# Optimization experiments

Measured on AMD Instinct MI355X. Metric: run time of the kernel, lower is better.

## Reference

```python
import jax, jax.numpy as jnp
import numpy as np

H = 32   # hidden_dim
D = 3    # input_dim
NM, NF = 16, 64
ME, FE = 4, 2


def setup_inputs() -> dict:
    key = jax.random.key(0)
    ks = jax.random.split(key, 12)
    B, T = 16384, 1024
    s_ih = 1.0 / np.sqrt(H)
    inp = {
        "x": jax.random.normal(ks[0], (B, T, D), dtype=jnp.float32),
        "mat_idx": jax.random.randint(ks[1], (B,), 0, NM, dtype=jnp.int32),
        "freq_idx": jax.random.randint(ks[2], (B,), 0, NF, dtype=jnp.int32),
        # LSTM params (PyTorch layout: gates [i, f, g, o] stacked)
        "W_ih": jax.random.uniform(ks[3], (4 * H, D), jnp.float32, -s_ih, s_ih),
        "W_hh": jax.random.uniform(ks[4], (4 * H, H), jnp.float32, -s_ih, s_ih),
        "b_ih": jax.random.uniform(ks[5], (4 * H,), jnp.float32, -s_ih, s_ih),
        "b_hh": jax.random.uniform(ks[6], (4 * H,), jnp.float32, -s_ih, s_ih),
        "mat_emb": jax.random.normal(ks[7], (NM, ME), dtype=jnp.float32),
        "freq_emb": jax.random.normal(ks[8], (NF, FE), dtype=jnp.float32),
        "fc_w": jax.random.uniform(ks[9], (1, H + ME + FE), jnp.float32, -s_ih, s_ih),
        "fc_b": jax.random.uniform(ks[10], (1,), jnp.float32, -s_ih, s_ih),
    }
    return inp


def _lstm_last(x, W_ih, W_hh, b_ih, b_hh):
    # x: [B, T, D] -> last hidden state h_T: [B, H]
    B = x.shape[0]
    # Precompute input projections for all timesteps: [T, B, 4H]
    xg = jnp.einsum("btd,gd->tbg", x, W_ih) + (b_ih + b_hh)

    def step(carry, xg_t):
        h, c = carry
        gates = xg_t + h @ W_hh.T  # [B, 4H]
        i, f, g, o = jnp.split(gates, 4, axis=-1)
        i, f, o = jax.nn.sigmoid(i), jax.nn.sigmoid(f), jax.nn.sigmoid(o)
        g = jnp.tanh(g)
        c = f * c + i * g
        h = o * jnp.tanh(c)
        return (h, c), None

    h0 = jnp.zeros((B, H), dtype=x.dtype)
    (h, _), _ = jax.lax.scan(step, (h0, h0), xg)
    return h


def reference(x, mat_idx, freq_idx, W_ih, W_hh, b_ih, b_hh,
              mat_emb, freq_emb, fc_w, fc_b):
    last = _lstm_last(x, W_ih, W_hh, b_ih, b_hh)          # [B, H]
    feat = jnp.concatenate(
        [last, mat_emb[mat_idx], freq_emb[freq_idx]], axis=-1)  # [B, H+ME+FE]
    return (feat @ fc_w.T + fc_b)[:, 0]                   # [B]
```

## Files before the change

kernel.cpp:

```cpp
#include <hip/hip_runtime.h>
#include <hip/hip_bf16.h>

#define H 32
#define DCT 32
#define BT 32
#define HPADB 80
#define XLDS_BYTES (DCT*32*16)
#define HLDS_OFF XLDS_BYTES
#define SMEM_BYTES (XLDS_BYTES + 32*HPADB)

typedef __attribute__((ext_vector_type(8))) short bfrag;
typedef __attribute__((ext_vector_type(4))) float ffrag;

__device__ __forceinline__ unsigned short f2bf(float f) {
  union { float f; unsigned u; } v; v.f = f;
  unsigned r = v.u + 0x7FFFu + ((v.u >> 16) & 1u);
  return (unsigned short)(r >> 16);
}

__device__ __forceinline__ float sigmoid_f(float x) {
  float e = __builtin_amdgcn_exp2f(x * -1.44269504f);
  return __builtin_amdgcn_rcpf(1.0f + e);
}
__device__ __forceinline__ float tanh_f(float x) {
  float e = __builtin_amdgcn_exp2f(x * 2.88539008f);
  return 1.0f - 2.0f * __builtin_amdgcn_rcpf(e + 1.0f);
}

__global__ __launch_bounds__(256, 2) void lstm_kernel(
    const float* __restrict__ x, const int* __restrict__ mat_idx,
    const int* __restrict__ freq_idx, const float* __restrict__ W_ih,
    const float* __restrict__ W_hh, const float* __restrict__ b_ih,
    const float* __restrict__ b_hh, const float* __restrict__ mat_emb,
    const float* __restrict__ freq_emb, const float* __restrict__ fc_w,
    const float* __restrict__ fc_b, float* __restrict__ out, int T)
{
  __shared__ __align__(16) unsigned char smem[SMEM_BYTES];
  const int tid  = threadIdx.x;
  const int lane = tid & 63;
  const int wid  = tid >> 6;
  const int mtile = wid & 1;
  const int h16   = wid >> 1;
  const int q    = lane >> 4;
  const int c16  = lane & 15;
  const int hid  = h16*16 + c16;
  const int b0   = blockIdx.x * BT;

  for (int i = tid; i < SMEM_BYTES/4; i += 256) ((unsigned*)smem)[i] = 0u;

  bfrag fw[4]; bfrag fx[4];
  #pragma unroll
  for (int g = 0; g < 4; ++g) {
    const int col = g*32 + hid;
    const float* wr = W_hh + col*H + q*8;
    #pragma unroll
    for (int j = 0; j < 8; ++j) fw[g][j] = (short)f2bf(wr[j]);
    #pragma unroll
    for (int j = 0; j < 8; ++j) {
      float v = 0.0f;
      if (q == 0) {
        if (j < 3)       v = W_ih[col*3 + j];
        else if (j == 3) v = b_ih[col] + b_hh[col];
      }
      fx[g][j] = (short)f2bf(v);
    }
  }

  const unsigned h_rd = HLDS_OFF + (unsigned)(mtile*16 + c16)*HPADB + q*16;
  const unsigned x_rd = (unsigned)(mtile*16 + c16)*16;

  float cc[4] = {0.f,0.f,0.f,0.f};
  float hh[4] = {0.f,0.f,0.f,0.f};

  const int srow = tid >> 3, ssub = tid & 7;
  const float* xsrc = x + (size_t)(b0 + srow) * (size_t)T * 3;

  for (int t0 = 0; t0 < T; t0 += DCT) {
    __syncthreads();
    {
      const float* p = xsrc + (size_t)(t0 + ssub*4) * 3;
      float v[12];
      #pragma unroll
      for (int u = 0; u < 12; ++u) v[u] = p[u];
      #pragma unroll
      for (int u = 0; u < 4; ++u) {
        unsigned w0 = (unsigned)f2bf(v[u*3+0]) | ((unsigned)f2bf(v[u*3+1]) << 16);
        unsigned w1 = (unsigned)f2bf(v[u*3+2]) | (0x3F80u << 16);
        unsigned* dst = (unsigned*)(smem + (unsigned)((ssub*4+u)*32 + srow)*16);
        dst[0] = w0; dst[1] = w1;
      }
    }
    __syncthreads();

    for (int tl = 0; tl < DCT; ++tl) {
      bfrag ah = *(const bfrag*)(smem + h_rd);
      bfrag ax = *(const bfrag*)(smem + (unsigned)tl*512 + x_rd);
      ffrag acc[4] = {};
      #pragma unroll
      for (int g = 0; g < 4; ++g) {
        acc[g] = __builtin_amdgcn_mfma_f32_16x16x32_bf16(ax, fx[g], acc[g], 0,0,0);
        acc[g] = __builtin_amdgcn_mfma_f32_16x16x32_bf16(ah, fw[g], acc[g], 0,0,0);
      }
      __syncthreads();
      #pragma unroll
      for (int r = 0; r < 4; ++r) {
        float ig = sigmoid_f(acc[0][r]);
        float fg = sigmoid_f(acc[1][r]);
        float gg = tanh_f(acc[2][r]);
        float og = sigmoid_f(acc[3][r]);
        float c  = fg*cc[r] + ig*gg;
        cc[r] = c;
        float h = og * tanh_f(c);
        hh[r] = h;
        *(unsigned short*)(smem + HLDS_OFF +
            (unsigned)(mtile*16 + q*4 + r)*HPADB + (unsigned)hid*2) = f2bf(h);
      }
      __syncthreads();
    }
  }

  __syncthreads();
  float* hout = (float*)smem;
  #pragma unroll
  for (int r = 0; r < 4; ++r)
    hout[(mtile*16 + q*4 + r)*H + hid] = hh[r];
  __syncthreads();
  if (tid < BT) {
    const int b = b0 + tid;
    float acc = fc_b[0];
    const float* hv = hout + tid*H;
    #pragma unroll
    for (int k = 0; k < H; ++k) acc += hv[k]*fc_w[k];
    const int mi = mat_idx[b];
    #pragma unroll
    for (int e = 0; e < 4; ++e) acc += mat_emb[mi*4+e]*fc_w[H+e];
    const int fi = freq_idx[b];
    #pragma unroll
    for (int e = 0; e < 2; ++e) acc += freq_emb[fi*2+e]*fc_w[H+4+e];
    out[b] = acc;
  }
}

extern "C" void kernel_launch(void* const* d_in, const int* in_sizes, int n_in,
                              void* d_out, int out_size, void* d_ws, size_t ws_size,
                              hipStream_t stream) {
  const float* x        = (const float*)d_in[0];
  const int*   mat_idx  = (const int*)d_in[1];
  const int*   freq_idx = (const int*)d_in[2];
  const float* W_ih     = (const float*)d_in[3];
  const float* W_hh     = (const float*)d_in[4];
  const float* b_ih     = (const float*)d_in[5];
  const float* b_hh     = (const float*)d_in[6];
  const float* mat_emb  = (const float*)d_in[7];
  const float* freq_emb = (const float*)d_in[8];
  const float* fc_w     = (const float*)d_in[9];
  const float* fc_b     = (const float*)d_in[10];
  float* out = (float*)d_out;
  const int B = in_sizes[1];
  const int T = in_sizes[0] / (B * 3);
  dim3 grid(B / BT), block(256);
  hipLaunchKernelGGL(lstm_kernel, grid, block, 0, stream,
                     x, mat_idx, freq_idx, W_ih, W_hh, b_ih, b_hh,
                     mat_emb, freq_emb, fc_w, fc_b, out, T);
}
```

Before: 923.7 us.

## Double-buffer LSTM hidden state, halve batch tile, prescale gate weights

Hidden-state LDS is double-buffered so each recurrent step needs one barrier instead of two. The batch tile drops from 32 to 16 rows with 128-thread blocks, doubling the number of independent blocks to hide the serial step latency. Gate weights and biases are pre-multiplied by the exp2 scale factors so the sigmoid and tanh evaluations skip a multiply per element. Prescaling before bf16 rounding slightly changes numerics, and smaller blocks reuse the weight fragments less.

```diff
diff --git a/kernel.cpp b/kernel.cpp
--- a/kernel.cpp
+++ b/kernel.cpp
@@ -3,11 +3,12 @@
 
 #define H 32
 #define DCT 32
-#define BT 32
+#define BT 16
 #define HPADB 80
-#define XLDS_BYTES (DCT*32*16)
+#define XLDS_BYTES (DCT*BT*16)
 #define HLDS_OFF XLDS_BYTES
-#define SMEM_BYTES (XLDS_BYTES + 32*HPADB)
+#define HBUF (BT*HPADB)
+#define SMEM_BYTES (XLDS_BYTES + 2*HBUF)
 
 typedef __attribute__((ext_vector_type(8))) short bfrag;
 typedef __attribute__((ext_vector_type(4))) float ffrag;
@@ -18,16 +19,45 @@
   return (unsigned short)(r >> 16);
 }
 
-__device__ __forceinline__ float sigmoid_f(float x) {
-  float e = __builtin_amdgcn_exp2f(x * -1.44269504f);
-  return __builtin_amdgcn_rcpf(1.0f + e);
+__device__ __forceinline__ float sig_pre(float s) {
+  return __builtin_amdgcn_rcpf(1.0f + __builtin_amdgcn_exp2f(s));
 }
-__device__ __forceinline__ float tanh_f(float x) {
-  float e = __builtin_amdgcn_exp2f(x * 2.88539008f);
-  return 1.0f - 2.0f * __builtin_amdgcn_rcpf(e + 1.0f);
+__device__ __forceinline__ float tanh_pre(float s) {
+  return 1.0f - 2.0f * __builtin_amdgcn_rcpf(1.0f + __builtin_amdgcn_exp2f(s));
 }
 
-__global__ __launch_bounds__(256, 2) void lstm_kernel(
+__device__ __forceinline__ void lstm_step(unsigned char* smem,
+    unsigned x_off, unsigned rd_off, unsigned wr_off,
+    const bfrag* fx, const bfrag* fw, ffrag fzero, float* cc, float* hh)
+{
+  bfrag ah = *(const bfrag*)(smem + rd_off);
+  bfrag ax = *(const bfrag*)(smem + x_off);
+  ffrag a0 = __builtin_amdgcn_mfma_f32_16x16x32_bf16(ax, fx[0], fzero, 0,0,0);
+  ffrag a1 = __builtin_amdgcn_mfma_f32_16x16x32_bf16(ax, fx[1], fzero, 0,0,0);
+  ffrag a2 = __builtin_amdgcn_mfma_f32_16x16x32_bf16(ax, fx[2], fzero, 0,0,0);
+  ffrag a3 = __builtin_amdgcn_mfma_f32_16x16x32_bf16(ax, fx[3], fzero, 0,0,0);
+  a0 = __builtin_amdgcn_mfma_f32_16x16x32_bf16(ah, fw[0], a0, 0,0,0);
+  a1 = __builtin_amdgcn_mfma_f32_16x16x32_bf16(ah, fw[1], a1, 0,0,0);
+  a2 = __builtin_amdgcn_mfma_f32_16x16x32_bf16(ah, fw[2], a2, 0,0,0);
+  a3 = __builtin_amdgcn_mfma_f32_16x16x32_bf16(ah, fw[3], a3, 0,0,0);
+  #pragma unroll
+  for (int r = 0; r < 4; ++r) {
+    float i_ = sig_pre(a0[r]);
+    float f_ = sig_pre(a1[r]);
+    float tg = tanh_pre(a2[r]);
+    float o_ = sig_pre(a3[r]);
+    float c  = f_*cc[r] + i_*tg;
+    cc[r] = c;
+    float h = o_ * tanh_pre(c * 2.885390082f);
+    hh[r] = h;
+    __hip_bfloat16 hb = __float2bfloat16(h);
+    *(unsigned short*)(smem + wr_off + (unsigned)r*HPADB) =
+        __builtin_bit_cast(unsigned short, hb);
+  }
+  __syncthreads();
+}
+
+__global__ __launch_bounds__(128, 2) void lstm_kernel(
     const float* __restrict__ x, const int* __restrict__ mat_idx,
     const int* __restrict__ freq_idx, const float* __restrict__ W_ih,
     const float* __restrict__ W_hh, const float* __restrict__ b_ih,
@@ -38,45 +68,49 @@
   __shared__ __align__(16) unsigned char smem[SMEM_BYTES];
   const int tid  = threadIdx.x;
   const int lane = tid & 63;
-  const int wid  = tid >> 6;
-  const int mtile = wid & 1;
-  const int h16   = wid >> 1;
+  const int h16  = tid >> 6;
   const int q    = lane >> 4;
   const int c16  = lane & 15;
   const int hid  = h16*16 + c16;
   const int b0   = blockIdx.x * BT;
 
-  for (int i = tid; i < SMEM_BYTES/4; i += 256) ((unsigned*)smem)[i] = 0u;
+  for (int i = tid; i < SMEM_BYTES/4; i += 128) ((unsigned*)smem)[i] = 0u;
 
   bfrag fw[4]; bfrag fx[4];
   #pragma unroll
   for (int g = 0; g < 4; ++g) {
-    const int col = g*32 + hid;
+    const float sc = (g == 2) ? 2.885390082f : -1.442695041f;
+    const int col = g*H + hid;
     const float* wr = W_hh + col*H + q*8;
     #pragma unroll
-    for (int j = 0; j < 8; ++j) fw[g][j] = (short)f2bf(wr[j]);
+    for (int j = 0; j < 8; ++j) fw[g][j] = (short)f2bf(wr[j] * sc);
     #pragma unroll
     for (int j = 0; j < 8; ++j) {
       float v = 0.0f;
       if (q == 0) {
-        if (j < 3)       v = W_ih[col*3 + j];
-        else if (j == 3) v = b_ih[col] + b_hh[col];
+        if (j < 3)       v = W_ih[col*3 + j] * sc;
+        else if (j == 3) v = (b_ih[col] + b_hh[col]) * sc;
       }
       fx[g][j] = (short)f2bf(v);
     }
   }
 
-  const unsigned h_rd = HLDS_OFF + (unsigned)(mtile*16 + c16)*HPADB + q*16;
-  const unsigned x_rd = (unsigned)(mtile*16 + c16)*16;
+  const unsigned rdA = HLDS_OFF + (unsigned)c16*HPADB + (unsigned)q*16;
+  const unsigned rdB = rdA + HBUF;
+  const unsigned wrA = HLDS_OFF + (unsigned)(q*4)*HPADB + (unsigned)hid*2;
+  const unsigned wrB = wrA + HBUF;
+  const unsigned x_rd = (unsigned)c16*16;
 
+  ffrag fzero = {0.f,0.f,0.f,0.f};
   float cc[4] = {0.f,0.f,0.f,0.f};
   float hh[4] = {0.f,0.f,0.f,0.f};
 
   const int srow = tid >> 3, ssub = tid & 7;
   const float* xsrc = x + (size_t)(b0 + srow) * (size_t)T * 3;
 
+  __syncthreads();
+
   for (int t0 = 0; t0 < T; t0 += DCT) {
-    __syncthreads();
     {
       const float* p = xsrc + (size_t)(t0 + ssub*4) * 3;
       float v[12];
@@ -86,44 +120,23 @@
       for (int u = 0; u < 4; ++u) {
         unsigned w0 = (unsigned)f2bf(v[u*3+0]) | ((unsigned)f2bf(v[u*3+1]) << 16);
         unsigned w1 = (unsigned)f2bf(v[u*3+2]) | (0x3F80u << 16);
-        unsigned* dst = (unsigned*)(smem + (unsigned)((ssub*4+u)*32 + srow)*16);
-        dst[0] = w0; dst[1] = w1;
+        uint2* dst = (uint2*)(smem + (unsigned)((ssub*4+u)*BT + srow)*16);
+        *dst = make_uint2(w0, w1);
       }
     }
     __syncthreads();
 
-    for (int tl = 0; tl < DCT; ++tl) {
-      bfrag ah = *(const bfrag*)(smem + h_rd);
-      bfrag ax = *(const bfrag*)(smem + (unsigned)tl*512 + x_rd);
-      ffrag acc[4] = {};
-      #pragma unroll
-      for (int g = 0; g < 4; ++g) {
-        acc[g] = __builtin_amdgcn_mfma_f32_16x16x32_bf16(ax, fx[g], acc[g], 0,0,0);
-        acc[g] = __builtin_amdgcn_mfma_f32_16x16x32_bf16(ah, fw[g], acc[g], 0,0,0);
-      }
-      __syncthreads();
-      #pragma unroll
-      for (int r = 0; r < 4; ++r) {
-        float ig = sigmoid_f(acc[0][r]);
-        float fg = sigmoid_f(acc[1][r]);
-        float gg = tanh_f(acc[2][r]);
-        float og = sigmoid_f(acc[3][r]);
-        float c  = fg*cc[r] + ig*gg;
-        cc[r] = c;
-        float h = og * tanh_f(c);
-        hh[r] = h;
-        *(unsigned short*)(smem + HLDS_OFF +
-            (unsigned)(mtile*16 + q*4 + r)*HPADB + (unsigned)hid*2) = f2bf(h);
-      }
-      __syncthreads();
+    #pragma unroll 2
+    for (int tl = 0; tl < DCT; tl += 2) {
+      lstm_step(smem, x_rd + (unsigned)tl*(BT*16),     rdA, wrB, fx, fw, fzero, cc, hh);
+      lstm_step(smem, x_rd + (unsigned)(tl+1)*(BT*16), rdB, wrA, fx, fw, fzero, cc, hh);
     }
   }
 
-  __syncthreads();
   float* hout = (float*)smem;
   #pragma unroll
   for (int r = 0; r < 4; ++r)
-    hout[(mtile*16 + q*4 + r)*H + hid] = hh[r];
+    hout[(q*4 + r)*H + hid] = hh[r];
   __syncthreads();
   if (tid < BT) {
     const int b = b0 + tid;
@@ -158,7 +171,7 @@
   float* out = (float*)d_out;
   const int B = in_sizes[1];
   const int T = in_sizes[0] / (B * 3);
-  dim3 grid(B / BT), block(256);
+  dim3 grid(B / BT), block(128);
   hipLaunchKernelGGL(lstm_kernel, grid, block, 0, stream,
                      x, mat_idx, freq_idx, W_ih, W_hh, b_ih, b_hh,
                      mat_emb, freq_emb, fc_w, fc_b, out, T);
```

Result: faster. 889.4 us (-3.7%).
